# Performance work log

Measured on AMD Instinct MI355X. Metric: run time of the kernel, lower is better.

Reference implementation:

```python
import jax, jax.numpy as jnp
import numpy as np

# model dims (match init_kwargs)
D = 1024      # input_dim
H = 4096      # hidden_dim
O = 1024      # expert_output_dim
E = 8         # num_experts
K = 2         # top_k


def setup_inputs() -> dict:
    key = jax.random.key(0)
    ks = jax.random.split(key, 8)
    B, S = 2, 2048
    x = jax.random.normal(ks[0], (B, S, D), dtype=jnp.float32)
    s = 0.02
    Wr = jax.random.normal(ks[1], (D, E), dtype=jnp.float32) * s
    br = jnp.zeros((E,), dtype=jnp.float32)
    W1 = jax.random.normal(ks[2], (E, D, H), dtype=jnp.float32) * s
    b1 = jnp.zeros((E, H), dtype=jnp.float32)
    W2 = jax.random.normal(ks[3], (E, H, O), dtype=jnp.float32) * s
    b2 = jnp.zeros((E, O), dtype=jnp.float32)
    return {"x": x, "Wr": Wr, "br": br, "W1": W1, "b1": b1, "W2": W2, "b2": b2}


def reference(x, Wr, br, W1, b1, W2, b2):
    B, S, _ = x.shape
    T = B * S
    xf = x.reshape(T, D)                                  # [T, D]
    logits = xf @ Wr + br                                 # [T, E]
    topk_logits, topk_idx = jax.lax.top_k(logits, K)      # [T, K]
    gates = jax.nn.softmax(topk_logits, axis=1)           # softmax over the K selected logits
    # scatter gates into a dense [T, E] matrix (top-k indices are unique per token)
    dense_gates = jnp.zeros((T, E), dtype=logits.dtype).at[
        jnp.arange(T)[:, None], topk_idx
    ].set(gates)
    # run every expert FFN densely, then combine with (mostly-zero) gates
    h = jax.nn.relu(jnp.einsum('td,edh->teh', xf, W1) + b1)   # [T, E, H]
    y = jnp.einsum('teh,eho->teo', h, W2) + b2                # [T, E, O]
    out = jnp.einsum('te,teo->to', dense_gates, y)            # [T, O]
    return out.reshape(B, S, O)
```

## Files before the change

### kernel.cpp

```cpp
#include <hip/hip_runtime.h>
#include <stdint.h>

#define KD 1024
#define KH 4096
#define KO 1024
#define KE 8
#define KT 4096

typedef unsigned short u16;
typedef __bf16 bf16x8 __attribute__((ext_vector_type(8)));
typedef unsigned short ushort8 __attribute__((ext_vector_type(8)));
typedef float floatx4 __attribute__((ext_vector_type(4)));

__device__ __forceinline__ u16 f2bf(float f) {
  unsigned u = __float_as_uint(f);
  u += 0x7fffu + ((u >> 16) & 1u);
  return (u16)(u >> 16);
}

__device__ __forceinline__ void glds16(const u16* g, u16* l) {
  __builtin_amdgcn_global_load_lds(
      (const __attribute__((address_space(1))) unsigned int*)(g),
      (__attribute__((address_space(3))) unsigned int*)(l), 16, 0, 0);
}

__global__ void cvt_x_k(const float* __restrict__ x, u16* __restrict__ xbf) {
  int i = blockIdx.x * blockDim.x + threadIdx.x;
  float4 v = ((const float4*)x)[i];
  union { u16 u[4]; uint2 v2; } o;
  o.u[0] = f2bf(v.x); o.u[1] = f2bf(v.y); o.u[2] = f2bf(v.z); o.u[3] = f2bf(v.w);
  ((uint2*)xbf)[i] = o.v2;
}

__global__ void transpose_k(const float* __restrict__ in, u16* __restrict__ out,
                            int R, int C) {
  __shared__ float tile[32][33];
  const int e = blockIdx.z;
  const float* I = in + (size_t)e * R * C;
  u16* Oo = out + (size_t)e * R * C;
  const int c0 = blockIdx.x * 32, r0 = blockIdx.y * 32;
  const int tx = threadIdx.x, ty = threadIdx.y;
#pragma unroll
  for (int i = 0; i < 4; i++) {
    int r = r0 + ty + i * 8;
    tile[ty + i * 8][tx] = I[(size_t)r * C + c0 + tx];
  }
  __syncthreads();
#pragma unroll
  for (int i = 0; i < 4; i++) {
    int c = c0 + ty + i * 8;
    Oo[(size_t)c * R + r0 + tx] = f2bf(tile[tx][ty + i * 8]);
  }
}

__global__ void router_k(const float* __restrict__ x, const float* __restrict__ Wr,
                         const float* __restrict__ br, int* __restrict__ eidx,
                         float2* __restrict__ gpair) {
  const int t = blockIdx.x;
  const int lane = threadIdx.x;
  const float* xr = x + (size_t)t * KD;
  double acc[KE];
#pragma unroll
  for (int e = 0; e < KE; e++) acc[e] = 0.0;
  for (int i = lane; i < KD; i += 64) {
    float xv = xr[i];
    const float* wr = Wr + i * KE;
#pragma unroll
    for (int e = 0; e < KE; e++) acc[e] += (double)xv * (double)wr[e];
  }
#pragma unroll
  for (int e = 0; e < KE; e++) {
#pragma unroll
    for (int m = 32; m > 0; m >>= 1) acc[e] += __shfl_xor(acc[e], m, 64);
  }
  if (lane == 0) {
    float l[KE];
#pragma unroll
    for (int e = 0; e < KE; e++) l[e] = (float)acc[e] + br[e];
    int i0 = 0;
#pragma unroll
    for (int e = 1; e < KE; e++) if (l[e] > l[i0]) i0 = e;
    int i1 = -1;
#pragma unroll
    for (int e = 0; e < KE; e++) {
      if (e == i0) continue;
      if (i1 < 0 || l[e] > l[i1]) i1 = e;
    }
    float g0 = 1.0f / (1.0f + expf(l[i1] - l[i0]));
    eidx[t] = i0 | (i1 << 4);
    gpair[t] = make_float2(g0, 1.0f - g0);
  }
}

__global__ __launch_bounds__(256) void bucket_k(const int* __restrict__ eidx,
                                                const float2* __restrict__ gp,
                                                int* __restrict__ cnt,
                                                int* __restrict__ tok,
                                                float* __restrict__ gat) {
  const int e = blockIdx.x;
  const int tid = threadIdx.x;
  const int t0 = tid * 16;
  int f[16]; float g[16]; int c = 0;
#pragma unroll
  for (int j = 0; j < 16; j++) {
    int pk = eidx[t0 + j];
    float2 gg = gp[t0 + j];
    int h0 = ((pk & 15) == e);
    int h1 = (((pk >> 4) & 15) == e);
    f[j] = h0 | h1;
    g[j] = h0 ? gg.x : gg.y;
    c += f[j];
  }
  __shared__ int sc[256];
  sc[tid] = c;
  __syncthreads();
  for (int d = 1; d < 256; d <<= 1) {
    int add = (tid >= d) ? sc[tid - d] : 0;
    __syncthreads();
    sc[tid] += add;
    __syncthreads();
  }
  int base = sc[tid] - c;
  if (tid == 0) cnt[e] = sc[255];
#pragma unroll
  for (int j = 0; j < 16; j++) {
    if (f[j]) {
      tok[(e << 12) + base] = t0 + j;
      gat[(e << 12) + base] = g[j];
      base++;
    }
  }
}

__global__ void offsets_k(const int* __restrict__ cnt, int* __restrict__ offs) {
  if (threadIdx.x == 0 && blockIdx.x == 0) {
    int s = 0;
#pragma unroll
    for (int e = 0; e < KE; e++) { offs[e] = s; s += cnt[e]; }
  }
}

__global__ __launch_bounds__(256) void gemm1_k(
    const u16* __restrict__ xbf, const u16* __restrict__ w1t,
    const float* __restrict__ b1, const int* __restrict__ cnt,
    const int* __restrict__ offs, const int* __restrict__ tok,
    u16* __restrict__ hbuf) {
  const int e = blockIdx.z;
  const int me = cnt[e];
  const int m0 = blockIdx.y * 128;
  if (m0 >= me) return;
  const int n0 = blockIdx.x * 128;
  const int oe = offs[e];
  const int* tk = tok + (e << 12);

  __shared__ u16 As[128 * 32];
  __shared__ u16 Bs[128 * 32];

  const int tid = threadIdx.x;
  const int lane = tid & 63;
  const int w = tid >> 6;
  const int wm = w >> 1, wn = w & 1;

  const int rr = lane >> 2;
  const int cc = (lane & 3) << 3;
  const int ar0 = m0 + w * 32 + rr;
  const int ar1 = ar0 + 16;
  const int ta0 = (ar0 < me) ? tk[ar0] : 0;
  const int ta1 = (ar1 < me) ? tk[ar1] : 0;
  const u16* ga0 = xbf + ((size_t)ta0 << 10) + cc;
  const u16* ga1 = xbf + ((size_t)ta1 << 10) + cc;
  const int br0 = n0 + w * 32 + rr;
  const u16* gb0 = w1t + ((size_t)e << 22) + ((size_t)br0 << 10) + cc;
  const u16* gb1 = gb0 + (16 << 10);
  u16* la0 = &As[(w * 32) * 32] + lane * 8;
  u16* la1 = la0 + 512;
  u16* lb0 = &Bs[(w * 32) * 32] + lane * 8;
  u16* lb1 = lb0 + 512;

  floatx4 acc[4][4] = {};
  const int fr = lane & 15;
  const int kq = (lane >> 4) << 3;

  for (int kt = 0; kt < KD / 32; ++kt) {
    __syncthreads();
    glds16(ga0 + kt * 32, la0);
    glds16(ga1 + kt * 32, la1);
    glds16(gb0 + kt * 32, lb0);
    glds16(gb1 + kt * 32, lb1);
    __builtin_amdgcn_s_waitcnt(0);
    __syncthreads();
    bf16x8 af[4], bfr[4];
#pragma unroll
    for (int i = 0; i < 4; i++) {
      af[i]  = __builtin_bit_cast(bf16x8, *(const ushort8*)&As[(wm * 64 + i * 16 + fr) * 32 + kq]);
      bfr[i] = __builtin_bit_cast(bf16x8, *(const ushort8*)&Bs[(wn * 64 + i * 16 + fr) * 32 + kq]);
    }
#pragma unroll
    for (int mi = 0; mi < 4; mi++)
#pragma unroll
      for (int ni = 0; ni < 4; ni++)
        acc[mi][ni] = __builtin_amdgcn_mfma_f32_16x16x32_bf16(af[mi], bfr[ni], acc[mi][ni], 0, 0, 0);
  }

  const int q = lane >> 4;
#pragma unroll
  for (int ni = 0; ni < 4; ni++) {
    const int gcol = n0 + wn * 64 + ni * 16 + fr;
    const float bb = b1[(e << 12) + gcol];
#pragma unroll
    for (int mi = 0; mi < 4; mi++) {
#pragma unroll
      for (int r = 0; r < 4; r++) {
        const int gr = m0 + wm * 64 + mi * 16 + q * 4 + r;
        if (gr < me) {
          float v = fmaxf(acc[mi][ni][r] + bb, 0.0f);
          hbuf[((size_t)(oe + gr) << 12) + gcol] = f2bf(v);
        }
      }
    }
  }
}

__global__ __launch_bounds__(256) void gemm2_k(
    const u16* __restrict__ hbuf, const u16* __restrict__ w2t,
    const float* __restrict__ b2, const int* __restrict__ cnt,
    const int* __restrict__ offs, const int* __restrict__ tok,
    const float* __restrict__ gat, float* __restrict__ out) {
  const int e = blockIdx.z;
  const int me = cnt[e];
  const int m0 = blockIdx.y * 128;
  if (m0 >= me) return;
  const int ks = blockIdx.x & 1;
  const int n0 = (blockIdx.x >> 1) * 128;
  const int k0 = ks * (KH / 2);
  const int oe = offs[e];
  const int* tk = tok + (e << 12);

  __shared__ u16 As[128 * 32];
  __shared__ u16 Bs[128 * 32];

  const int tid = threadIdx.x;
  const int lane = tid & 63;
  const int w = tid >> 6;
  const int wm = w >> 1, wn = w & 1;

  const int rr = lane >> 2;
  const int cc = (lane & 3) << 3;
  const int ar0 = m0 + w * 32 + rr;
  const int ar1 = ar0 + 16;
  const int sl0 = oe + ((ar0 < me) ? ar0 : 0);
  const int sl1 = oe + ((ar1 < me) ? ar1 : 0);
  const u16* ga0 = hbuf + ((size_t)sl0 << 12) + k0 + cc;
  const u16* ga1 = hbuf + ((size_t)sl1 << 12) + k0 + cc;
  const int br0 = n0 + w * 32 + rr;
  const u16* gb0 = w2t + ((size_t)e << 22) + ((size_t)br0 << 12) + k0 + cc;
  const u16* gb1 = gb0 + (16 << 12);
  u16* la0 = &As[(w * 32) * 32] + lane * 8;
  u16* la1 = la0 + 512;
  u16* lb0 = &Bs[(w * 32) * 32] + lane * 8;
  u16* lb1 = lb0 + 512;

  floatx4 acc[4][4] = {};
  const int fr = lane & 15;
  const int kq = (lane >> 4) << 3;

  for (int kt = 0; kt < KH / 2 / 32; ++kt) {
    __syncthreads();
    glds16(ga0 + kt * 32, la0);
    glds16(ga1 + kt * 32, la1);
    glds16(gb0 + kt * 32, lb0);
    glds16(gb1 + kt * 32, lb1);
    __builtin_amdgcn_s_waitcnt(0);
    __syncthreads();
    bf16x8 af[4], bfr[4];
#pragma unroll
    for (int i = 0; i < 4; i++) {
      af[i]  = __builtin_bit_cast(bf16x8, *(const ushort8*)&As[(wm * 64 + i * 16 + fr) * 32 + kq]);
      bfr[i] = __builtin_bit_cast(bf16x8, *(const ushort8*)&Bs[(wn * 64 + i * 16 + fr) * 32 + kq]);
    }
#pragma unroll
    for (int mi = 0; mi < 4; mi++)
#pragma unroll
      for (int ni = 0; ni < 4; ni++)
        acc[mi][ni] = __builtin_amdgcn_mfma_f32_16x16x32_bf16(af[mi], bfr[ni], acc[mi][ni], 0, 0, 0);
  }

  const int q = lane >> 4;
  float bb[4];
#pragma unroll
  for (int ni = 0; ni < 4; ni++)
    bb[ni] = (ks == 0) ? b2[(e << 10) + n0 + wn * 64 + ni * 16 + fr] : 0.0f;
#pragma unroll
  for (int mi = 0; mi < 4; mi++) {
#pragma unroll
    for (int r = 0; r < 4; r++) {
      const int gr = m0 + wm * 64 + mi * 16 + q * 4 + r;
      if (gr < me) {
        const int tt = tk[gr];
        const float g = gat[(e << 12) + gr];
        float* orow = out + ((size_t)tt << 10);
#pragma unroll
        for (int ni = 0; ni < 4; ni++) {
          const int gcol = n0 + wn * 64 + ni * 16 + fr;
          atomicAdd(orow + gcol, (acc[mi][ni][r] + bb[ni]) * g);
        }
      }
    }
  }
}

extern "C" void kernel_launch(void* const* d_in, const int* in_sizes, int n_in,
                              void* d_out, int out_size, void* d_ws, size_t ws_size,
                              hipStream_t stream) {
  const float* x  = (const float*)d_in[0];
  const float* Wr = (const float*)d_in[1];
  const float* br = (const float*)d_in[2];
  const float* W1 = (const float*)d_in[3];
  const float* b1 = (const float*)d_in[4];
  const float* W2 = (const float*)d_in[5];
  const float* b2 = (const float*)d_in[6];
  float* out = (float*)d_out;

  char* ws = (char*)d_ws;
  size_t p = 0;
  auto alloc = [&](size_t bytes) {
    void* r = ws + p;
    p = (p + bytes + 255) & ~(size_t)255;
    return r;
  };
  int*    cnt   = (int*)alloc(KE * 4);
  int*    offs  = (int*)alloc(KE * 4);
  int*    eidx  = (int*)alloc((size_t)KT * 4);
  float2* gpair = (float2*)alloc((size_t)KT * 8);
  int*    tok   = (int*)alloc((size_t)KE * KT * 4);
  float*  gat   = (float*)alloc((size_t)KE * KT * 4);
  u16*    xbf   = (u16*)alloc((size_t)KT * KD * 2);
  u16*    w1t   = (u16*)alloc((size_t)KE * KD * KH * 2);
  u16*    w2t   = (u16*)alloc((size_t)KE * KH * KO * 2);
  u16*    hbuf  = (u16*)alloc((size_t)2 * KT * KH * 2);

  hipMemsetAsync(out, 0, (size_t)KT * KO * 4, stream);

  cvt_x_k<<<(KT * KD / 4) / 256, 256, 0, stream>>>(x, xbf);
  transpose_k<<<dim3(KH / 32, KD / 32, KE), dim3(32, 8), 0, stream>>>(W1, w1t, KD, KH);
  transpose_k<<<dim3(KO / 32, KH / 32, KE), dim3(32, 8), 0, stream>>>(W2, w2t, KH, KO);
  router_k<<<KT, 64, 0, stream>>>(x, Wr, br, eidx, gpair);
  bucket_k<<<KE, 256, 0, stream>>>(eidx, gpair, cnt, tok, gat);
  offsets_k<<<1, 64, 0, stream>>>(cnt, offs);
  gemm1_k<<<dim3(KH / 128, KT / 128, KE), 256, 0, stream>>>(xbf, w1t, b1, cnt, offs, tok, hbuf);
  gemm2_k<<<dim3(2 * KO / 128, KT / 128, KE), 256, 0, stream>>>(hbuf, w2t, b2, cnt, offs, tok, gat, out);
}
```

Before: 620.4 us.

## Replace atomic scatter with split-K buffer and combine kernel; widen transpose and K-tile

gemm2 no longer scatters gated results into the output with float atomics. It writes its two split-K partial results into a dense buffer (reusing the w1t workspace, which is dead after gemm1). A new combine kernel then sums the partials, adds the bias, applies the gates per token, and writes the output once, so the memset and the atomic contention go away. The weight transpose now uses 64x64 tiles with float4 loads and 16-byte stores, and both GEMMs load 64-wide K chunks per barrier to halve the number of synchronizations. This adds an extra kernel and a larger fp32 intermediate round-trip, and doubles the LDS used by each GEMM block.

Result: no change. 608.4 us (-1.9%).

```diff
diff --git a/kernel.cpp b/kernel.cpp
--- a/kernel.cpp
+++ b/kernel.cpp
@@ -32,24 +32,32 @@
   ((uint2*)xbf)[i] = o.v2;
 }
 
-__global__ void transpose_k(const float* __restrict__ in, u16* __restrict__ out,
-                            int R, int C) {
-  __shared__ float tile[32][33];
+__global__ __launch_bounds__(256) void transpose_k(const float* __restrict__ in,
+                                                   u16* __restrict__ out, int R, int C) {
+  __shared__ float tile[64][65];
   const int e = blockIdx.z;
   const float* I = in + (size_t)e * R * C;
   u16* Oo = out + (size_t)e * R * C;
-  const int c0 = blockIdx.x * 32, r0 = blockIdx.y * 32;
-  const int tx = threadIdx.x, ty = threadIdx.y;
-#pragma unroll
-  for (int i = 0; i < 4; i++) {
-    int r = r0 + ty + i * 8;
-    tile[ty + i * 8][tx] = I[(size_t)r * C + c0 + tx];
+  const int c0 = blockIdx.x * 64, r0 = blockIdx.y * 64;
+  const int t = threadIdx.x;
+  const int rr = t >> 4;
+  const int c4 = (t & 15) << 2;
+#pragma unroll
+  for (int j = 0; j < 4; j++) {
+    int r = rr + j * 16;
+    float4 v = *(const float4*)&I[(size_t)(r0 + r) * C + c0 + c4];
+    tile[r][c4] = v.x; tile[r][c4 + 1] = v.y; tile[r][c4 + 2] = v.z; tile[r][c4 + 3] = v.w;
   }
   __syncthreads();
-#pragma unroll
-  for (int i = 0; i < 4; i++) {
-    int c = c0 + ty + i * 8;
-    Oo[(size_t)c * R + r0 + tx] = f2bf(tile[tx][ty + i * 8]);
+  const int cc = t >> 3;
+  const int rb = (t & 7) << 3;
+#pragma unroll
+  for (int j = 0; j < 2; j++) {
+    int c = cc + j * 32;
+    ushort8 o;
+#pragma unroll
+    for (int k = 0; k < 8; k++) o[k] = f2bf(tile[rb + k][c]);
+    *(ushort8*)&Oo[(size_t)(c0 + c) * R + r0 + rb] = o;
   }
 }
 
@@ -93,23 +101,20 @@
 }
 
 __global__ __launch_bounds__(256) void bucket_k(const int* __restrict__ eidx,
-                                                const float2* __restrict__ gp,
                                                 int* __restrict__ cnt,
                                                 int* __restrict__ tok,
-                                                float* __restrict__ gat) {
+                                                int* __restrict__ pos) {
   const int e = blockIdx.x;
   const int tid = threadIdx.x;
   const int t0 = tid * 16;
-  int f[16]; float g[16]; int c = 0;
+  int f[16]; int c = 0;
 #pragma unroll
   for (int j = 0; j < 16; j++) {
     int pk = eidx[t0 + j];
-    float2 gg = gp[t0 + j];
     int h0 = ((pk & 15) == e);
     int h1 = (((pk >> 4) & 15) == e);
-    f[j] = h0 | h1;
-    g[j] = h0 ? gg.x : gg.y;
-    c += f[j];
+    f[j] = h0 ? 1 : (h1 ? 2 : 0);
+    c += (f[j] != 0);
   }
   __shared__ int sc[256];
   sc[tid] = c;
@@ -126,7 +131,7 @@
   for (int j = 0; j < 16; j++) {
     if (f[j]) {
       tok[(e << 12) + base] = t0 + j;
-      gat[(e << 12) + base] = g[j];
+      pos[2 * (t0 + j) + (f[j] - 1)] = base;
       base++;
     }
   }
@@ -153,8 +158,8 @@
   const int oe = offs[e];
   const int* tk = tok + (e << 12);
 
-  __shared__ u16 As[128 * 32];
-  __shared__ u16 Bs[128 * 32];
+  __shared__ u16 As[2 * 128 * 32];
+  __shared__ u16 Bs[2 * 128 * 32];
 
   const int tid = threadIdx.x;
   const int lane = tid & 63;
@@ -172,34 +177,46 @@
   const int br0 = n0 + w * 32 + rr;
   const u16* gb0 = w1t + ((size_t)e << 22) + ((size_t)br0 << 10) + cc;
   const u16* gb1 = gb0 + (16 << 10);
-  u16* la0 = &As[(w * 32) * 32] + lane * 8;
-  u16* la1 = la0 + 512;
-  u16* lb0 = &Bs[(w * 32) * 32] + lane * 8;
-  u16* lb1 = lb0 + 512;
+  u16* la00 = &As[w * 1024] + lane * 8;
+  u16* la01 = la00 + 512;
+  u16* la10 = la00 + 4096;
+  u16* la11 = la00 + 4096 + 512;
+  u16* lb00 = &Bs[w * 1024] + lane * 8;
+  u16* lb01 = lb00 + 512;
+  u16* lb10 = lb00 + 4096;
+  u16* lb11 = lb00 + 4096 + 512;
 
   floatx4 acc[4][4] = {};
   const int fr = lane & 15;
   const int kq = (lane >> 4) << 3;
 
-  for (int kt = 0; kt < KD / 32; ++kt) {
-    __syncthreads();
-    glds16(ga0 + kt * 32, la0);
-    glds16(ga1 + kt * 32, la1);
-    glds16(gb0 + kt * 32, lb0);
-    glds16(gb1 + kt * 32, lb1);
+  for (int kt = 0; kt < KD / 64; ++kt) {
+    const int k64 = kt * 64;
+    __syncthreads();
+    glds16(ga0 + k64,      la00);
+    glds16(ga1 + k64,      la01);
+    glds16(ga0 + k64 + 32, la10);
+    glds16(ga1 + k64 + 32, la11);
+    glds16(gb0 + k64,      lb00);
+    glds16(gb1 + k64,      lb01);
+    glds16(gb0 + k64 + 32, lb10);
+    glds16(gb1 + k64 + 32, lb11);
     __builtin_amdgcn_s_waitcnt(0);
     __syncthreads();
-    bf16x8 af[4], bfr[4];
-#pragma unroll
-    for (int i = 0; i < 4; i++) {
-      af[i]  = __builtin_bit_cast(bf16x8, *(const ushort8*)&As[(wm * 64 + i * 16 + fr) * 32 + kq]);
-      bfr[i] = __builtin_bit_cast(bf16x8, *(const ushort8*)&Bs[(wn * 64 + i * 16 + fr) * 32 + kq]);
-    }
-#pragma unroll
-    for (int mi = 0; mi < 4; mi++)
-#pragma unroll
-      for (int ni = 0; ni < 4; ni++)
-        acc[mi][ni] = __builtin_amdgcn_mfma_f32_16x16x32_bf16(af[mi], bfr[ni], acc[mi][ni], 0, 0, 0);
+#pragma unroll
+    for (int p = 0; p < 2; p++) {
+      bf16x8 af[4], bfr[4];
+#pragma unroll
+      for (int i = 0; i < 4; i++) {
+        af[i]  = __builtin_bit_cast(bf16x8, *(const ushort8*)&As[p * 4096 + (wm * 64 + i * 16 + fr) * 32 + kq]);
+        bfr[i] = __builtin_bit_cast(bf16x8, *(const ushort8*)&Bs[p * 4096 + (wn * 64 + i * 16 + fr) * 32 + kq]);
+      }
+#pragma unroll
+      for (int mi = 0; mi < 4; mi++)
+#pragma unroll
+        for (int ni = 0; ni < 4; ni++)
+          acc[mi][ni] = __builtin_amdgcn_mfma_f32_16x16x32_bf16(af[mi], bfr[ni], acc[mi][ni], 0, 0, 0);
+    }
   }
 
   const int q = lane >> 4;
@@ -223,9 +240,8 @@
 
 __global__ __launch_bounds__(256) void gemm2_k(
     const u16* __restrict__ hbuf, const u16* __restrict__ w2t,
-    const float* __restrict__ b2, const int* __restrict__ cnt,
-    const int* __restrict__ offs, const int* __restrict__ tok,
-    const float* __restrict__ gat, float* __restrict__ out) {
+    const int* __restrict__ cnt, const int* __restrict__ offs,
+    float* __restrict__ y) {
   const int e = blockIdx.z;
   const int me = cnt[e];
   const int m0 = blockIdx.y * 128;
@@ -234,10 +250,9 @@
   const int n0 = (blockIdx.x >> 1) * 128;
   const int k0 = ks * (KH / 2);
   const int oe = offs[e];
-  const int* tk = tok + (e << 12);
-
-  __shared__ u16 As[128 * 32];
-  __shared__ u16 Bs[128 * 32];
+
+  __shared__ u16 As[2 * 128 * 32];
+  __shared__ u16 Bs[2 * 128 * 32];
 
   const int tid = threadIdx.x;
   const int lane = tid & 63;
@@ -255,58 +270,89 @@
   const int br0 = n0 + w * 32 + rr;
   const u16* gb0 = w2t + ((size_t)e << 22) + ((size_t)br0 << 12) + k0 + cc;
   const u16* gb1 = gb0 + (16 << 12);
-  u16* la0 = &As[(w * 32) * 32] + lane * 8;
-  u16* la1 = la0 + 512;
-  u16* lb0 = &Bs[(w * 32) * 32] + lane * 8;
-  u16* lb1 = lb0 + 512;
+  u16* la00 = &As[w * 1024] + lane * 8;
+  u16* la01 = la00 + 512;
+  u16* la10 = la00 + 4096;
+  u16* la11 = la00 + 4096 + 512;
+  u16* lb00 = &Bs[w * 1024] + lane * 8;
+  u16* lb01 = lb00 + 512;
+  u16* lb10 = lb00 + 4096;
+  u16* lb11 = lb00 + 4096 + 512;
 
   floatx4 acc[4][4] = {};
   const int fr = lane & 15;
   const int kq = (lane >> 4) << 3;
 
-  for (int kt = 0; kt < KH / 2 / 32; ++kt) {
-    __syncthreads();
-    glds16(ga0 + kt * 32, la0);
-    glds16(ga1 + kt * 32, la1);
-    glds16(gb0 + kt * 32, lb0);
-    glds16(gb1 + kt * 32, lb1);
+  for (int kt = 0; kt < KH / 2 / 64; ++kt) {
+    const int k64 = kt * 64;
+    __syncthreads();
+    glds16(ga0 + k64,      la00);
+    glds16(ga1 + k64,      la01);
+    glds16(ga0 + k64 + 32, la10);
+    glds16(ga1 + k64 + 32, la11);
+    glds16(gb0 + k64,      lb00);
+    glds16(gb1 + k64,      lb01);
+    glds16(gb0 + k64 + 32, lb10);
+    glds16(gb1 + k64 + 32, lb11);
     __builtin_amdgcn_s_waitcnt(0);
     __syncthreads();
-    bf16x8 af[4], bfr[4];
-#pragma unroll
-    for (int i = 0; i < 4; i++) {
-      af[i]  = __builtin_bit_cast(bf16x8, *(const ushort8*)&As[(wm * 64 + i * 16 + fr) * 32 + kq]);
-      bfr[i] = __builtin_bit_cast(bf16x8, *(const ushort8*)&Bs[(wn * 64 + i * 16 + fr) * 32 + kq]);
-    }
-#pragma unroll
-    for (int mi = 0; mi < 4; mi++)
-#pragma unroll
-      for (int ni = 0; ni < 4; ni++)
-        acc[mi][ni] = __builtin_amdgcn_mfma_f32_16x16x32_bf16(af[mi], bfr[ni], acc[mi][ni], 0, 0, 0);
+#pragma unroll
+    for (int p = 0; p < 2; p++) {
+      bf16x8 af[4], bfr[4];
+#pragma unroll
+      for (int i = 0; i < 4; i++) {
+        af[i]  = __builtin_bit_cast(bf16x8, *(const ushort8*)&As[p * 4096 + (wm * 64 + i * 16 + fr) * 32 + kq]);
+        bfr[i] = __builtin_bit_cast(bf16x8, *(const ushort8*)&Bs[p * 4096 + (wn * 64 + i * 16 + fr) * 32 + kq]);
+      }
+#pragma unroll
+      for (int mi = 0; mi < 4; mi++)
+#pragma unroll
+        for (int ni = 0; ni < 4; ni++)
+          acc[mi][ni] = __builtin_amdgcn_mfma_f32_16x16x32_bf16(af[mi], bfr[ni], acc[mi][ni], 0, 0, 0);
+    }
   }
 
   const int q = lane >> 4;
-  float bb[4];
-#pragma unroll
-  for (int ni = 0; ni < 4; ni++)
-    bb[ni] = (ks == 0) ? b2[(e << 10) + n0 + wn * 64 + ni * 16 + fr] : 0.0f;
+  float* yk = y + ((size_t)ks << 23);
 #pragma unroll
   for (int mi = 0; mi < 4; mi++) {
 #pragma unroll
     for (int r = 0; r < 4; r++) {
       const int gr = m0 + wm * 64 + mi * 16 + q * 4 + r;
       if (gr < me) {
-        const int tt = tk[gr];
-        const float g = gat[(e << 12) + gr];
-        float* orow = out + ((size_t)tt << 10);
-#pragma unroll
-        for (int ni = 0; ni < 4; ni++) {
-          const int gcol = n0 + wn * 64 + ni * 16 + fr;
-          atomicAdd(orow + gcol, (acc[mi][ni][r] + bb[ni]) * g);
-        }
+        float* yrow = yk + ((size_t)(oe + gr) << 10);
+#pragma unroll
+        for (int ni = 0; ni < 4; ni++)
+          yrow[n0 + wn * 64 + ni * 16 + fr] = acc[mi][ni][r];
       }
     }
   }
+}
+
+__global__ __launch_bounds__(256) void combine_k(
+    const float* __restrict__ y, const int* __restrict__ eidx,
+    const float2* __restrict__ gp, const int* __restrict__ offs,
+    const int* __restrict__ pos, const float* __restrict__ b2,
+    float* __restrict__ out) {
+  const int t = blockIdx.x;
+  const int c4 = threadIdx.x << 2;
+  const int pk = eidx[t];
+  const int e0 = pk & 15, e1 = (pk >> 4) & 15;
+  const float2 g = gp[t];
+  const int s0 = offs[e0] + pos[2 * t];
+  const int s1 = offs[e1] + pos[2 * t + 1];
+  float4 a0 = *(const float4*)(y + ((size_t)s0 << 10) + c4);
+  float4 a1 = *(const float4*)(y + (1ull << 23) + ((size_t)s0 << 10) + c4);
+  float4 c0 = *(const float4*)(y + ((size_t)s1 << 10) + c4);
+  float4 c1 = *(const float4*)(y + (1ull << 23) + ((size_t)s1 << 10) + c4);
+  float4 ba = *(const float4*)(b2 + (e0 << 10) + c4);
+  float4 bc = *(const float4*)(b2 + (e1 << 10) + c4);
+  float4 o;
+  o.x = g.x * (a0.x + a1.x + ba.x) + g.y * (c0.x + c1.x + bc.x);
+  o.y = g.x * (a0.y + a1.y + ba.y) + g.y * (c0.y + c1.y + bc.y);
+  o.z = g.x * (a0.z + a1.z + ba.z) + g.y * (c0.z + c1.z + bc.z);
+  o.w = g.x * (a0.w + a1.w + ba.w) + g.y * (c0.w + c1.w + bc.w);
+  *(float4*)(out + ((size_t)t << 10) + c4) = o;
 }
 
 extern "C" void kernel_launch(void* const* d_in, const int* in_sizes, int n_in,
@@ -332,21 +378,21 @@
   int*    offs  = (int*)alloc(KE * 4);
   int*    eidx  = (int*)alloc((size_t)KT * 4);
   float2* gpair = (float2*)alloc((size_t)KT * 8);
+  int*    pos   = (int*)alloc((size_t)2 * KT * 4);
   int*    tok   = (int*)alloc((size_t)KE * KT * 4);
-  float*  gat   = (float*)alloc((size_t)KE * KT * 4);
   u16*    xbf   = (u16*)alloc((size_t)KT * KD * 2);
   u16*    w1t   = (u16*)alloc((size_t)KE * KD * KH * 2);
   u16*    w2t   = (u16*)alloc((size_t)KE * KH * KO * 2);
   u16*    hbuf  = (u16*)alloc((size_t)2 * KT * KH * 2);
-
-  hipMemsetAsync(out, 0, (size_t)KT * KO * 4, stream);
+  float*  y     = (float*)w1t;
 
   cvt_x_k<<<(KT * KD / 4) / 256, 256, 0, stream>>>(x, xbf);
-  transpose_k<<<dim3(KH / 32, KD / 32, KE), dim3(32, 8), 0, stream>>>(W1, w1t, KD, KH);
-  transpose_k<<<dim3(KO / 32, KH / 32, KE), dim3(32, 8), 0, stream>>>(W2, w2t, KH, KO);
+  transpose_k<<<dim3(KH / 64, KD / 64, KE), 256, 0, stream>>>(W1, w1t, KD, KH);
+  transpose_k<<<dim3(KO / 64, KH / 64, KE), 256, 0, stream>>>(W2, w2t, KH, KO);
   router_k<<<KT, 64, 0, stream>>>(x, Wr, br, eidx, gpair);
-  bucket_k<<<KE, 256, 0, stream>>>(eidx, gpair, cnt, tok, gat);
+  bucket_k<<<KE, 256, 0, stream>>>(eidx, cnt, tok, pos);
   offsets_k<<<1, 64, 0, stream>>>(cnt, offs);
   gemm1_k<<<dim3(KH / 128, KT / 128, KE), 256, 0, stream>>>(xbf, w1t, b1, cnt, offs, tok, hbuf);
-  gemm2_k<<<dim3(2 * KO / 128, KT / 128, KE), 256, 0, stream>>>(hbuf, w2t, b2, cnt, offs, tok, gat, out);
-}
+  gemm2_k<<<dim3(2 * KO / 128, KT / 128, KE), 256, 0, stream>>>(hbuf, w2t, cnt, offs, y);
+  combine_k<<<KT, 256, 0, stream>>>(y, eidx, gpair, offs, pos, b2, out);
+}
```
